# Performance work log

Measured on AMD Instinct MI355X. Metric: run time of the kernel, lower is better.

The kernel has to match this reference:

```python
import jax, jax.numpy as jnp
import numpy as np

B, C, N, L = 64, 32, 500, 12
C_OUT = 32
C_CAT = 9 * C  # (order*(support_len+1)+1)*c_in = 288


def setup_inputs() -> dict:
    key = jax.random.key(0)
    ks = jax.random.split(key, 7)
    x = jax.random.normal(ks[0], (B, C, N, L), dtype=jnp.float32)
    # row-stochastic-ish adjacencies: scale by 1/N to keep hops numerically tame
    A0 = jax.random.uniform(ks[1], (N, N), dtype=jnp.float32) / N
    A1 = jax.random.uniform(ks[2], (N, N), dtype=jnp.float32) / N
    A2 = jax.random.uniform(ks[3], (N, N), dtype=jnp.float32) / N
    A3 = jax.random.uniform(ks[4], (B, N, N), dtype=jnp.float32) / N
    W = jax.random.normal(ks[5], (C_OUT, C_CAT), dtype=jnp.float32) * 0.05
    b = jax.random.normal(ks[6], (C_OUT,), dtype=jnp.float32) * 0.05
    return {"x": x, "A0": A0, "A1": A1, "A2": A2, "A3": A3, "W": W, "b": b}


def reference(x, A0, A1, A2, A3, W, b):
    # x: [B, C, N, L]; A0..A2: [N, N]; A3: [B, N, N]; W: [C_OUT, 9*C]; b: [C_OUT]
    def hop2(h, A):  # static adjacency
        return jnp.einsum('ncvl,vw->ncwl', h, A)

    def hop3(h, A):  # batched (dynamic) adjacency
        return jnp.einsum('ncvl,nvw->ncwl', h, A)

    out = [x]
    for A in (A0, A1, A2):
        x1 = hop2(x, A)
        x2 = hop2(x1, A)
        out.extend([x1, x2])
    x1 = hop3(x, A3)
    x2 = hop3(x1, A3)
    out.extend([x1, x2])

    h = jnp.concatenate(out, axis=1)  # [B, 9C, N, L]
    # 1x1 Conv2d == channel mixing matmul + bias
    h = jnp.einsum('ncvl,oc->novl', h, W) + b[None, :, None, None]
    # dropout in eval mode: identity
    return h
```

## Files before the change

kernel.cpp:

```cpp
#include <hip/hip_runtime.h>

typedef unsigned short u16;
typedef __bf16 bf16x8 __attribute__((ext_vector_type(8)));
typedef float f32x4 __attribute__((ext_vector_type(4)));
typedef const unsigned int __attribute__((address_space(1))) gu32;
typedef unsigned int __attribute__((address_space(3))) lu32;

#define NN 500
#define LLc 12
#define CC 32
#define MM 384
#define KP 512
#define MT 96
#define NT2 128
#define XS_S 40
#define AS_S 40
#define CT2_S 136
#define TS_S 384
#define AT_ELS 256000

__device__ __forceinline__ u16 f2bf(float f) {
    union { float f; unsigned u; } cv; cv.f = f;
    unsigned u = cv.u;
    u += 0x7fffu + ((u >> 16) & 1u);
    return (u16)(u >> 16);
}
__device__ __forceinline__ float bf2f(u16 s) {
    union { unsigned u; float f; } cv; cv.u = ((unsigned)s) << 16;
    return cv.f;
}

__global__ __launch_bounds__(256) void atrans_all(
    const float* __restrict__ A0, const float* __restrict__ A1,
    const float* __restrict__ A2, const float* __restrict__ A3,
    u16* __restrict__ At_s, u16* __restrict__ At_b)
{
    __shared__ u16 Ls[32 * 36];
    const int t = threadIdx.x;
    const int n0 = blockIdx.x * 32;
    const int k0 = blockIdx.y * 32;
    const int z = blockIdx.z;
    const float* Ab; u16* Ob;
    if (z == 0)      { Ab = A0; Ob = At_s; }
    else if (z == 1) { Ab = A1; Ob = At_s + (long)AT_ELS; }
    else if (z == 2) { Ab = A2; Ob = At_s + 2L * AT_ELS; }
    else             { Ab = A3 + (long)(z - 3) * NN * NN; Ob = At_b + (long)(z - 3) * AT_ELS; }
    {
        int vl = t >> 3, u = t & 7;
        float4 v = make_float4(0.f, 0.f, 0.f, 0.f);
        if (k0 + vl < NN && n0 + 4 * u + 4 <= NN)
            v = *(const float4*)(Ab + (long)(k0 + vl) * NN + n0 + 4 * u);
        int nb = 4 * u;
        Ls[(nb + 0) * 36 + vl] = f2bf(v.x);
        Ls[(nb + 1) * 36 + vl] = f2bf(v.y);
        Ls[(nb + 2) * 36 + vl] = f2bf(v.z);
        Ls[(nb + 3) * 36 + vl] = f2bf(v.w);
    }
    __syncthreads();
    {
        int row = t >> 3, u = t & 7;
        if (n0 + row < NN)
            *(uint2*)(Ob + (long)(n0 + row) * KP + k0 + 4 * u) = *(const uint2*)(&Ls[row * 36 + 4 * u]);
    }
}

__global__ __launch_bounds__(256) void xpose_kernel(
    const float* __restrict__ x, u16* __restrict__ Xt)
{
    __shared__ u16 Ls[MM * 36];
    const int t = threadIdx.x;
    const int v0 = blockIdx.x * 32;
    const int b  = blockIdx.y;
    #pragma unroll
    for (int j = 0; j < 12; ++j) {
        int f = t + 256 * j;
        int c = f / 96;
        int r = f - c * 96;
        int vl = r / 3;
        int l3 = (r - vl * 3) * 4;
        float4 v = make_float4(0.f, 0.f, 0.f, 0.f);
        if (v0 + vl < NN)
            v = *(const float4*)(x + ((long)b * CC + c) * (NN * LLc) + (long)(v0 + vl) * LLc + l3);
        int mb = (c * LLc + l3) * 36 + vl;
        Ls[mb]       = f2bf(v.x);
        Ls[mb + 36]  = f2bf(v.y);
        Ls[mb + 72]  = f2bf(v.z);
        Ls[mb + 108] = f2bf(v.w);
    }
    __syncthreads();
    #pragma unroll
    for (int j = 0; j < 12; ++j) {
        int f = t + 256 * j;
        int row = f >> 3, u = f & 7;
        *(uint2*)(Xt + ((long)b * MM + row) * KP + v0 + 4 * u) = *(const uint2*)(&Ls[row * 36 + 4 * u]);
    }
}

__global__ __launch_bounds__(256) void wpack_kernel(
    const float* __restrict__ W, u16* __restrict__ Wp)
{
    const int t = threadIdx.x;
    #pragma unroll 1
    for (int k = 0; k < 72; ++k) {
        int idx = t + 256 * k;
        int j    = idx & 7;
        int lane = (idx >> 3) & 63;
        int p    = (idx >> 9) & 1;
        int mt   = (idx >> 10) & 1;
        int g    = idx >> 11;
        int o  = mt * 16 + (lane & 15);
        int kk = g * 32 + (lane >> 4) * 8 + j;
        float wv = W[o * 288 + kk];
        u16 hi = f2bf(wv);
        Wp[idx] = (p == 0) ? hi : f2bf(wv - bf2f(hi));
    }
}

__global__ __launch_bounds__(256, 3) void hop_fast4(
    const u16* __restrict__ Xsrc, long x_gstride, long x_bstride,
    const u16* __restrict__ At_s,
    const u16* __restrict__ At_b,
    u16* __restrict__ Hout, long h_gstride)
{
    __shared__ __align__(16) u16 smem[20480];
    u16* Ct = smem;

    const int t = threadIdx.x;
    const int lane = t & 63;
    const int wv = t >> 6;
    const int f0 = blockIdx.x + 4 * blockIdx.y + 8 * blockIdx.z;
    const int w  = (f0 & 7) * 256 + (f0 >> 3);
    const int bx = w & 3;
    const int by = (w >> 2) & 1;
    const int zc = w >> 3;
    const int g  = zc & 3;
    const int b  = zc >> 2;
    const int n0 = bx * NT2;
    const int m0 = by * 192;
    const int ln  = lane & 15;
    const int q16 = lane >> 4;

    const u16* Ab = (g < 3) ? (At_s + (long)g * AT_ELS) : (At_b + (long)b * AT_ELS);
    const u16* Xb = Xsrc + (long)g * x_gstride + (long)b * x_bstride;
    u16* Ob = Hout + (long)g * h_gstride + (long)b * ((long)MM * KP);

    const int rbase = lane >> 2;
    const int coff  = (((lane & 3) ^ ((lane >> 3) & 3)) << 3);
    const int rsel  = ((q16 ^ ((ln >> 1) & 3)) << 3);

    auto STAGE = [&](int kk, int pb) {
        #pragma unroll
        for (int j = 0; j < 5; ++j) {
            int o = (wv * 5 + j) << 10;
            const u16* src;
            if (o < 8192) {
                src = Ab + (long)(n0 + (o >> 6) + rbase) * KP + kk + coff;
            } else {
                src = Xb + (long)(m0 + (o >> 6) - 128 + rbase) * KP + kk + coff;
            }
            __builtin_amdgcn_global_load_lds((gu32*)src,
                (lu32*)((char*)smem + pb * 20480 + o), 16, 0, 0);
        }
    };

    f32x4 acc[2][12];
    #pragma unroll
    for (int ns = 0; ns < 2; ++ns)
        #pragma unroll
        for (int i = 0; i < 12; ++i)
            #pragma unroll
            for (int r = 0; r < 4; ++r) acc[ns][i][r] = 0.f;

    STAGE(0, 0);
    asm volatile("s_waitcnt vmcnt(0)" ::: "memory");
    __syncthreads();

    #pragma unroll 1
    for (int s = 0; s < 16; ++s) {
        const int pb = s & 1;
        if (s < 15) STAGE(32 * (s + 1), pb ^ 1);
        const u16* As = smem + pb * 10240;
        const u16* Xs = As + 4096;
        const int rowA0 = wv * 32 + ln;
        bf16x8 b0 = *(const bf16x8*)(&As[rowA0 * 32 + rsel]);
        bf16x8 b1 = *(const bf16x8*)(&As[(rowA0 + 16) * 32 + rsel]);
        #pragma unroll
        for (int i = 0; i < 12; ++i) {
            bf16x8 af = *(const bf16x8*)(&Xs[(i * 16 + ln) * 32 + rsel]);
            acc[0][i] = __builtin_amdgcn_mfma_f32_16x16x32_bf16(af, b0, acc[0][i], 0, 0, 0);
            acc[1][i] = __builtin_amdgcn_mfma_f32_16x16x32_bf16(af, b1, acc[1][i], 0, 0, 0);
        }
        asm volatile("s_waitcnt vmcnt(0)" ::: "memory");
        __syncthreads();
    }

    #pragma unroll
    for (int h = 0; h < 2; ++h) {
        __syncthreads();
        #pragma unroll
        for (int ns = 0; ns < 2; ++ns) {
            int col = wv * 32 + ns * 16 + ln;
            #pragma unroll
            for (int i6 = 0; i6 < 6; ++i6) {
                int rb = i6 * 16 + (lane >> 4) * 4;
                #pragma unroll
                for (int r = 0; r < 4; ++r)
                    Ct[(rb + r) * CT2_S + col] = f2bf(acc[ns][h * 6 + i6][r]);
            }
        }
        __syncthreads();
        #pragma unroll
        for (int j = 0; j < 12; ++j) {
            int f = t + 256 * j;
            int row = f >> 5, u = f & 31;
            int n = n0 + 4 * u;
            uint2 v = make_uint2(0u, 0u);
            if (n < NN) v = *(const uint2*)(&Ct[row * CT2_S + 4 * u]);
            *(uint2*)(Ob + (long)(m0 + h * 96 + row) * KP + n) = v;
        }
    }
}

__global__ __launch_bounds__(256, 3) void hop_fast3(
    const u16* __restrict__ Xsrc, long x_gstride, long x_bstride, int x_rstride, int x_klim,
    const u16* __restrict__ At_s,
    const u16* __restrict__ At_b,
    u16* __restrict__ Hout, long h_gstride)
{
    __shared__ __align__(16) u16 smem[13056];
    u16* As = smem;
    u16* Xs = smem + 5120;
    u16* Ct = smem;

    const int t = threadIdx.x;
    const int lane = t & 63;
    const int wv = t >> 6;
    const int f0 = blockIdx.x + 4 * blockIdx.y + 8 * blockIdx.z;
    const int w  = (f0 & 7) * 256 + (f0 >> 3);
    const int bx = w & 3;
    const int by = (w >> 2) & 1;
    const int zc = w >> 3;
    const int g  = zc & 3;
    const int b  = zc >> 2;
    const int n0 = bx * NT2;
    const int m0 = by * 192;
    const int ln = lane & 15;
    const int q8 = (lane >> 4) * 8;

    const u16* Ab = (g < 3) ? (At_s + (long)g * AT_ELS) : (At_b + (long)b * AT_ELS);
    const u16* Xb = Xsrc + (long)g * x_gstride + (long)b * x_bstride;
    u16* Ob = Hout + (long)g * h_gstride + (long)b * ((long)MM * NN);

    uint2 pa[4], px[6];
    auto loadA = [&](int k0) {
        #pragma unroll
        for (int j = 0; j < 4; ++j) {
            int f = t + 256 * j;
            int n = f >> 3, u = f & 7;
            uint2 v = make_uint2(0u, 0u);
            if (n0 + n < NN)
                v = *(const uint2*)(Ab + (long)(n0 + n) * KP + k0 + 4 * u);
            pa[j] = v;
        }
    };
    auto loadX = [&](int k0) {
        #pragma unroll
        for (int j = 0; j < 6; ++j) {
            int f = t + 256 * j;
            int r = f >> 3, u = f & 7;
            int k = k0 + 4 * u;
            uint2 v = make_uint2(0u, 0u);
            if (k < x_klim)
                v = *(const uint2*)(Xb + (long)(m0 + r) * x_rstride + k);
            px[j] = v;
        }
    };

    f32x4 acc[2][12];
    #pragma unroll
    for (int ns = 0; ns < 2; ++ns)
        #pragma unroll
        for (int i = 0; i < 12; ++i)
            #pragma unroll
            for (int r = 0; r < 4; ++r) acc[ns][i][r] = 0.f;

    loadA(0);
    loadX(0);
    #pragma unroll 1
    for (int s = 0; s < 16; ++s) {
        __syncthreads();
        #pragma unroll
        for (int j = 0; j < 4; ++j) {
            int f = t + 256 * j;
            *(uint2*)(&As[(f >> 3) * AS_S + 4 * (f & 7)]) = pa[j];
        }
        #pragma unroll
        for (int j = 0; j < 6; ++j) {
            int f = t + 256 * j;
            *(uint2*)(&Xs[(f >> 3) * XS_S + 4 * (f & 7)]) = px[j];
        }
        if (s < 15) {
            loadA(32 * (s + 1));
            loadX(32 * (s + 1));
        }
        __syncthreads();
        bf16x8 b0 = *(const bf16x8*)(&As[(wv * 32 + ln) * AS_S + q8]);
        bf16x8 b1 = *(const bf16x8*)(&As[(wv * 32 + 16 + ln) * AS_S + q8]);
        #pragma unroll
        for (int i = 0; i < 12; ++i) {
            bf16x8 af = *(const bf16x8*)(&Xs[(i * 16 + ln) * XS_S + q8]);
            acc[0][i] = __builtin_amdgcn_mfma_f32_16x16x32_bf16(af, b0, acc[0][i], 0, 0, 0);
            acc[1][i] = __builtin_amdgcn_mfma_f32_16x16x32_bf16(af, b1, acc[1][i], 0, 0, 0);
        }
    }

    #pragma unroll
    for (int h = 0; h < 2; ++h) {
        __syncthreads();
        #pragma unroll
        for (int ns = 0; ns < 2; ++ns) {
            int col = wv * 32 + ns * 16 + ln;
            #pragma unroll
            for (int i6 = 0; i6 < 6; ++i6) {
                int rb = i6 * 16 + (lane >> 4) * 4;
                #pragma unroll
                for (int r = 0; r < 4; ++r)
                    Ct[(rb + r) * CT2_S + col] = f2bf(acc[ns][h * 6 + i6][r]);
            }
        }
        __syncthreads();
        #pragma unroll
        for (int j = 0; j < 12; ++j) {
            int f = t + 256 * j;
            int row = f >> 5, u = f & 31;
            int n = n0 + 4 * u;
            if (n < NN)
                *(uint2*)(Ob + (long)(m0 + h * 96 + row) * NN + n) = *(const uint2*)(&Ct[row * CT2_S + 4 * u]);
        }
    }
}

__global__ __launch_bounds__(512, 4) void mix_mfma(
    const u16* __restrict__ Xt,
    const u16* __restrict__ H,
    const u16* __restrict__ Wp,
    const float* __restrict__ bias,
    float* __restrict__ out,
    long h_gs, long h_bs, int h_rs)
{
    __shared__ __align__(16) char smem[50176];
    u16*   Ls = (u16*)smem;
    float* Ct = (float*)smem;

    const int t   = threadIdx.x;
    const int wg  = blockIdx.y * 8 + blockIdx.x;
    const int swz = (wg & 7) * 64 + (wg >> 3);
    const int bx  = swz & 7;
    const int b   = swz >> 3;
    const int n0  = bx * 64;
    const int w    = t >> 6;
    const int lane = t & 63;
    const int kq   = lane >> 4;
    const int ln   = lane & 15;
    const int srow   = lane >> 3;
    const int schunk = (lane & 7) * 8;

    f32x4 acc[6][2];
    #pragma unroll
    for (int i = 0; i < 6; ++i)
        #pragma unroll
        for (int m = 0; m < 2; ++m)
            #pragma unroll
            for (int r = 0; r < 4; ++r) acc[i][m][r] = 0.f;

    #pragma unroll 1
    for (int g = 0; g < 9; ++g) {
        const u16* base; int rs;
        if (g == 0) { base = Xt + (long)b * (MM * KP); rs = KP; }
        else {
            int gg = g - 1;
            int buf = (gg & 1) ? 4 + (gg >> 1) : (gg >> 1);
            base = H + (long)buf * h_gs + (long)b * h_bs; rs = h_rs;
        }
        __syncthreads();
        #pragma unroll
        for (int i = 0; i < 6; ++i) {
            int r0 = (w * 6 + i) * 8;
            const u16* src = base + (long)(r0 + srow) * rs + n0 + schunk;
            __builtin_amdgcn_global_load_lds((gu32*)src, (lu32*)(Ls + r0 * 64), 16, 0, 0);
        }
        asm volatile("s_waitcnt vmcnt(0)" ::: "memory");
        __syncthreads();
        uint4 wf[2][2];
        #pragma unroll
        for (int mt = 0; mt < 2; ++mt)
            #pragma unroll
            for (int p = 0; p < 2; ++p)
                wf[mt][p] = *(const uint4*)(Wp + ((((g * 2 + mt) * 2 + p) * 64 + lane) * 8));
        #pragma unroll
        for (int i = 0; i < 6; ++i) {
            int ct = w * 6 + i;
            int off0 = kq * 6144 + (ct >> 2) * 64 + (ct & 3) * 16 + ln;
            union { u16 s[8]; bf16x8 v; } fb;
            #pragma unroll
            for (int j = 0; j < 8; ++j) fb.s[j] = Ls[off0 + j * 768];
            #pragma unroll
            for (int mt = 0; mt < 2; ++mt) {
                acc[i][mt] = __builtin_amdgcn_mfma_f32_16x16x32_bf16(*(const bf16x8*)&wf[mt][0], fb.v, acc[i][mt], 0, 0, 0);
                acc[i][mt] = __builtin_amdgcn_mfma_f32_16x16x32_bf16(*(const bf16x8*)&wf[mt][1], fb.v, acc[i][mt], 0, 0, 0);
            }
        }
    }

    #pragma unroll
    for (int mt = 0; mt < 2; ++mt) {
        __syncthreads();
        #pragma unroll
        for (int i = 0; i < 6; ++i) {
            int col = (w * 6 + i) * 16 + ln;
            #pragma unroll
            for (int r = 0; r < 4; ++r)
                Ct[(kq * 4 + r) * 781 + col] = acc[i][mt][r];
        }
        __syncthreads();
        int o16 = t >> 5, u = t & 31;
        int og = mt * 16 + o16;
        float bs = bias[og];
        float* ob = out + (((long)b * CC + og) * NN + n0) * 12L;
        #pragma unroll
        for (int j2 = 0; j2 < 2; ++j2) {
            int n = u + 32 * j2;
            if (n0 + n < NN) {
                float v[12];
                #pragma unroll
                for (int l = 0; l < 12; ++l) v[l] = Ct[o16 * 781 + l * 64 + n] + bs;
                #pragma unroll
                for (int q = 0; q < 3; ++q)
                    *(float4*)(ob + (long)n * 12 + q * 4) = *(const float4*)&v[q * 4];
            }
        }
    }
}

__global__ __launch_bounds__(256, 3) void mix_all(
    const u16* __restrict__ Xt,
    const u16* __restrict__ H,
    const float* __restrict__ W,
    const float* __restrict__ bias,
    float* __restrict__ out)
{
    __shared__ __align__(16) float smem[96 * 36 + 288 * 33];
    float* ts = smem;
    float* Ws = smem + 96 * 36;

    const int t  = threadIdx.x;
    const int b  = blockIdx.y;
    const int w0 = blockIdx.x * 32;
    const int o  = t & 31;
    const int wq = t >> 5;
    const int w4 = wq * 4;
    const long HBUF = (long)64 * MM * NN;

    #pragma unroll
    for (int j = 0; j < 36; ++j) {
        int f = t + 256 * j;
        int oo = f & 31, ci = f >> 5;
        Ws[ci * 33 + oo] = W[oo * 288 + ci];
    }

    float acc[4][12];
    #pragma unroll
    for (int k = 0; k < 4; ++k)
        #pragma unroll
        for (int l = 0; l < 12; ++l) acc[k][l] = 0.f;

    uint2 px[3];
    auto loadq = [&](int q) {
        int g = q >> 2, c0 = (q & 3) << 3;
        const u16* base; int rs;
        if (g == 0) { base = Xt + (long)b * (MM * KP); rs = KP; }
        else {
            int gg = g - 1, i = gg >> 1;
            int buf = (gg & 1) ? 4 + i : i;
            base = H + (long)buf * HBUF + (long)b * ((long)MM * NN); rs = NN;
        }
        int m0c = c0 * 12;
        #pragma unroll
        for (int j = 0; j < 3; ++j) {
            int f = t + 256 * j;
            int r = f >> 3, u = f & 7;
            px[j] = *(const uint2*)(base + (long)(m0c + r) * rs + w0 + 4 * u);
        }
    };

    loadq(0);
    #pragma unroll 1
    for (int q = 0; q < 36; ++q) {
        __syncthreads();
        #pragma unroll
        for (int j = 0; j < 3; ++j) {
            int f = t + 256 * j;
            int r = f >> 3, u = f & 7;
            uint2 raw = px[j];
            float4 v = make_float4(bf2f((u16)(raw.x & 0xffffu)), bf2f((u16)(raw.x >> 16)),
                                   bf2f((u16)(raw.y & 0xffffu)), bf2f((u16)(raw.y >> 16)));
            *(float4*)(&ts[r * 36 + 4 * u]) = v;
        }
        if (q < 35) loadq(q + 1);
        __syncthreads();
        int g = q >> 2, c0 = (q & 3) << 3;
        #pragma unroll 1
        for (int cl = 0; cl < 8; ++cl) {
            float wgt = Ws[(g * 32 + c0 + cl) * 33 + o];
            #pragma unroll
            for (int l = 0; l < 12; ++l) {
                float4 h = *(const float4*)(&ts[(cl * 12 + l) * 36 + w4]);
                acc[0][l] += wgt * h.x;
                acc[1][l] += wgt * h.y;
                acc[2][l] += wgt * h.z;
                acc[3][l] += wgt * h.w;
            }
        }
    }

    #pragma unroll 1
    for (int r = 0; r < 4; ++r) {
        __syncthreads();
        if ((o >> 3) == r) {
            int ol = o & 7;
            #pragma unroll
            for (int k = 0; k < 4; ++k)
                #pragma unroll
                for (int l = 0; l < 12; ++l)
                    ts[ol * 388 + (w4 + k) * 12 + l] = acc[k][l];
        }
        __syncthreads();
        #pragma unroll
        for (int j = 0; j < 3; ++j) {
            int f4 = t + 256 * j;
            int ol = f4 / 96;
            int rem = f4 - ol * 96;
            int w  = rem / 3;
            int lq = rem - w * 3;
            if (w0 + w < NN) {
                float4 v = *(const float4*)(&ts[ol * 388 + w * 12 + lq * 4]);
                float bs = bias[r * 8 + ol];
                v.x += bs; v.y += bs; v.z += bs; v.w += bs;
                *(float4*)(out + (((long)b * CC + r * 8 + ol) * NN + w0 + w) * LLc + lq * 4) = v;
            }
        }
    }
}

__global__ __launch_bounds__(256, 4) void hop_fast(
    const u16* __restrict__ Xsrc, long x_bstride, int x_rstride, int x_klim,
    const u16* __restrict__ At,   long a_bstride,
    u16* __restrict__ hout)
{
    __shared__ __align__(16) u16 smem[13056];
    u16* As = smem;
    u16* Xs = smem + 5120;
    u16* Ct = smem;

    const int t = threadIdx.x;
    const int lane = t & 63;
    const int wv = t >> 6;
    const int n0 = blockIdx.x * NT2;
    const int m0 = blockIdx.y * MT;
    const int b  = blockIdx.z;
    const int ln = lane & 15;
    const int q8 = (lane >> 4) * 8;

    const u16* Ab = At + (long)b * a_bstride;
    const u16* Xb = Xsrc + (long)b * x_bstride;

    uint2 pa[4], px[3];
    auto loadA = [&](int k0) {
        #pragma unroll
        for (int j = 0; j < 4; ++j) {
            int f = t + 256 * j;
            int n = f >> 3, u = f & 7;
            uint2 v = make_uint2(0u, 0u);
            if (n0 + n < NN)
                v = *(const uint2*)(Ab + (long)(n0 + n) * KP + k0 + 4 * u);
            pa[j] = v;
        }
    };
    auto loadX = [&](int k0) {
        #pragma unroll
        for (int j = 0; j < 3; ++j) {
            int f = t + 256 * j;
            int r = f >> 3, u = f & 7;
            int k = k0 + 4 * u;
            uint2 v = make_uint2(0u, 0u);
            if (k < x_klim)
                v = *(const uint2*)(Xb + (long)(m0 + r) * x_rstride + k);
            px[j] = v;
        }
    };

    f32x4 acc[2][6];
    #pragma unroll
    for (int ns = 0; ns < 2; ++ns)
        #pragma unroll
        for (int i = 0; i < 6; ++i)
            #pragma unroll
            for (int r = 0; r < 4; ++r) acc[ns][i][r] = 0.f;

    loadA(0);
    loadX(0);
    #pragma unroll 1
    for (int s = 0; s < 16; ++s) {
        __syncthreads();
        #pragma unroll
        for (int j = 0; j < 4; ++j) {
            int f = t + 256 * j;
            *(uint2*)(&As[(f >> 3) * AS_S + 4 * (f & 7)]) = pa[j];
        }
        #pragma unroll
        for (int j = 0; j < 3; ++j) {
            int f = t + 256 * j;
            *(uint2*)(&Xs[(f >> 3) * XS_S + 4 * (f & 7)]) = px[j];
        }
        if (s < 15) {
            loadA(32 * (s + 1));
            loadX(32 * (s + 1));
        }
        __syncthreads();
        bf16x8 af[6];
        #pragma unroll
        for (int i = 0; i < 6; ++i)
            af[i] = *(const bf16x8*)(&Xs[(i * 16 + ln) * XS_S + q8]);
        #pragma unroll
        for (int ns = 0; ns < 2; ++ns) {
            bf16x8 bfr = *(const bf16x8*)(&As[(wv * 32 + ns * 16 + ln) * AS_S + q8]);
            #pragma unroll
            for (int i = 0; i < 6; ++i)
                acc[ns][i] = __builtin_amdgcn_mfma_f32_16x16x32_bf16(af[i], bfr, acc[ns][i], 0, 0, 0);
        }
    }

    __syncthreads();
    #pragma unroll
    for (int ns = 0; ns < 2; ++ns) {
        int col = wv * 32 + ns * 16 + ln;
        #pragma unroll
        for (int i = 0; i < 6; ++i) {
            int rb = i * 16 + (lane >> 4) * 4;
            #pragma unroll
            for (int r = 0; r < 4; ++r)
                Ct[(rb + r) * CT2_S + col] = f2bf(acc[ns][i][r]);
        }
    }
    __syncthreads();
    u16* Ob = hout + (long)b * ((long)MM * NN);
    #pragma unroll
    for (int j = 0; j < 12; ++j) {
        int f = t + 256 * j;
        int row = f >> 5, u = f & 31;
        int n = n0 + 4 * u;
        if (n < NN)
            *(uint2*)(Ob + (long)(m0 + row) * NN + n) = *(const uint2*)(&Ct[row * CT2_S + 4 * u]);
    }
}

__global__ __launch_bounds__(256, 2) void mix_kernel(
    const float* __restrict__ x,
    const u16* __restrict__ h1,
    const u16* __restrict__ h2,
    const float* __restrict__ W,
    const float* __restrict__ bias,
    int blk1, int blk2,
    float* __restrict__ out, int init)
{
    __shared__ __align__(16) float smem[CC * TS_S + 3 * 1056];
    float* ts = smem;
    float* Ws = smem + CC * TS_S;

    const int t = threadIdx.x;
    const int b = blockIdx.y;
    const int w0 = blockIdx.x * 32;
    const int o  = t & 15;
    const int wg = (t >> 4) & 7;
    const int lh = t >> 7;

    #pragma unroll
    for (int j = 0; j < 4; ++j) {
        int f = t + 256 * j;
        int oo = f & 31, c = f >> 5;
        Ws[c * 33 + oo]        = W[oo * 288 + blk1 * 32 + c];
        Ws[1056 + c * 33 + oo] = W[oo * 288 + blk2 * 32 + c];
        if (init) Ws[2112 + c * 33 + oo] = W[oo * 288 + c];
    }

    float acc2[2][4][6];
    #pragma unroll
    for (int a = 0; a < 2; ++a)
        #pragma unroll
        for (int q = 0; q < 4; ++q)
            #pragma unroll
            for (int l = 0; l < 6; ++l) acc2[a][q][l] = 0.f;

    auto stage_h = [&](const u16* h) {
        #pragma unroll
        for (int j = 0; j < 12; ++j) {
            int f = t + 256 * j;
            int row = f >> 3, u = f & 7;
            int w = w0 + 4 * u;
            uint2 raw = make_uint2(0u, 0u);
            if (w < NN)
                raw = *(const uint2*)(h + ((long)b * MM + row) * NN + w);
            int c = row / 12;
            int l = row - c * 12;
            float* dst = &ts[c * TS_S + l * 32 + 4 * u];
            dst[0] = bf2f((u16)(raw.x & 0xffffu));
            dst[1] = bf2f((u16)(raw.x >> 16));
            dst[2] = bf2f((u16)(raw.y & 0xffffu));
            dst[3] = bf2f((u16)(raw.y >> 16));
        }
    };
    auto accum = [&](const float* Wg) {
        for (int c = 0; c < CC; ++c) {
            float w1 = Wg[c * 33 + o];
            float w2 = Wg[c * 33 + o + 16];
            #pragma unroll
            for (int l6 = 0; l6 < 6; ++l6) {
                const float4 hv = *(const float4*)(&ts[c * TS_S + (lh * 6 + l6) * 32 + wg * 4]);
                acc2[0][0][l6] += w1 * hv.x;
                acc2[0][1][l6] += w1 * hv.y;
                acc2[0][2][l6] += w1 * hv.z;
                acc2[0][3][l6] += w1 * hv.w;
                acc2[1][0][l6] += w2 * hv.x;
                acc2[1][1][l6] += w2 * hv.y;
                acc2[1][2][l6] += w2 * hv.z;
                acc2[1][3][l6] += w2 * hv.w;
            }
        }
    };

    if (init) {
        #pragma unroll
        for (int j = 0; j < 12; ++j) {
            int f = t + 256 * j;
            int c = f / 96;
            int r = f - c * 96;
            int w = r / 3;
            int q = r - w * 3;
            float4 v = make_float4(0.f, 0.f, 0.f, 0.f);
            if (w0 + w < NN)
                v = *(const float4*)(x + ((long)b * CC + c) * (NN * LLc) + (long)(w0 + w) * LLc + q * 4);
            float* dst = &ts[c * TS_S + (q * 4) * 32 + w];
            dst[0]  = v.x; dst[32] = v.y; dst[64] = v.z; dst[96] = v.w;
        }
        __syncthreads();
        accum(Ws + 2112);
        __syncthreads();
    }
    stage_h(h1);
    __syncthreads();
    accum(Ws);
    __syncthreads();
    stage_h(h2);
    __syncthreads();
    accum(Ws + 1056);

    #pragma unroll
    for (int oh = 0; oh < 2; ++oh) {
        int oo = o + 16 * oh;
        float bs = init ? bias[oo] : 0.f;
        #pragma unroll
        for (int q = 0; q < 4; ++q) {
            int w = w0 + wg * 4 + q;
            if (w < NN) {
                float* op = out + ((long)b * CC + oo) * (NN * LLc) + (long)w * LLc + lh * 6;
                #pragma unroll
                for (int p = 0; p < 3; ++p) {
                    float2* pp = (float2*)op + p;
                    float2 v;
                    if (init) {
                        v.x = bs + acc2[oh][q][2 * p];
                        v.y = bs + acc2[oh][q][2 * p + 1];
                    } else {
                        v = *pp;
                        v.x += acc2[oh][q][2 * p];
                        v.y += acc2[oh][q][2 * p + 1];
                    }
                    *pp = v;
                }
            }
        }
    }
}

extern "C" void kernel_launch(void* const* d_in, const int* in_sizes, int n_in,
                              void* d_out, int out_size, void* d_ws, size_t ws_size,
                              hipStream_t stream) {
    const float* x    = (const float*)d_in[0];
    const float* A0   = (const float*)d_in[1];
    const float* A1   = (const float*)d_in[2];
    const float* A2   = (const float*)d_in[3];
    const float* A3   = (const float*)d_in[4];
    const float* W    = (const float*)d_in[5];
    const float* bias = (const float*)d_in[6];
    float* out = (float*)d_out;
    char* ws = (char*)d_ws;

    const size_t HBUF_ELS  = (size_t)64 * MM * NN;
    const size_t H8_BYTES  = 8 * HBUF_ELS * 2;
    const size_t AT_BYTES  = (size_t)AT_ELS * 2;
    const size_t A3T_BYTES = 64 * AT_BYTES;
    const size_t XT_BYTES  = (size_t)64 * MM * KP * 2;
    const size_t need2 = H8_BYTES + 3 * AT_BYTES + A3T_BYTES + XT_BYTES;
    const size_t WPK_BYTES = 36864;
    const size_t need3 = need2 + WPK_BYTES;
    const size_t HB2_ELS  = (size_t)64 * MM * KP;
    const size_t H8B_PAD  = 8 * HB2_ELS * 2;
    const size_t need4 = H8B_PAD + 3 * AT_BYTES + A3T_BYTES + XT_BYTES + WPK_BYTES;

    dim3 blk(256);
    dim3 hgrid(4, 2, 256);

    if (ws_size >= need4) {
        u16* Hb   = (u16*)ws;
        u16* At_s = (u16*)(ws + H8B_PAD);
        u16* A3t  = At_s + 3L * AT_ELS;
        u16* Xt   = (u16*)(ws + H8B_PAD + 3 * AT_BYTES + A3T_BYTES);
        u16* Wpk  = Xt + (size_t)64 * MM * KP;

        atrans_all<<<dim3(16, 16, 67), blk, 0, stream>>>(A0, A1, A2, A3, At_s, A3t);
        xpose_kernel<<<dim3(16, 64), blk, 0, stream>>>(x, Xt);
        wpack_kernel<<<dim3(1), blk, 0, stream>>>(W, Wpk);
        hop_fast4<<<hgrid, blk, 0, stream>>>(
            Xt, 0L, (long)MM * KP, At_s, A3t, Hb, (long)HB2_ELS);
        hop_fast4<<<hgrid, blk, 0, stream>>>(
            Hb, (long)HB2_ELS, (long)MM * KP, At_s, A3t,
            Hb + 4 * HB2_ELS, (long)HB2_ELS);
        mix_mfma<<<dim3(8, 64), dim3(512), 0, stream>>>(
            Xt, Hb, Wpk, bias, out, (long)HB2_ELS, (long)MM * KP, KP);
        return;
    }

    if (ws_size >= need3) {
        u16* Hb   = (u16*)ws;
        u16* At_s = (u16*)(ws + H8_BYTES);
        u16* A3t  = At_s + 3L * AT_ELS;
        u16* Xt   = (u16*)(ws + H8_BYTES + 3 * AT_BYTES + A3T_BYTES);
        u16* Wpk  = (u16*)(ws + need2);

        atrans_all<<<dim3(16, 16, 67), blk, 0, stream>>>(A0, A1, A2, A3, At_s, A3t);
        xpose_kernel<<<dim3(16, 64), blk, 0, stream>>>(x, Xt);
        wpack_kernel<<<dim3(1), blk, 0, stream>>>(W, Wpk);
        hop_fast3<<<hgrid, blk, 0, stream>>>(
            Xt, 0L, (long)MM * KP, KP, KP, At_s, A3t, Hb, (long)HBUF_ELS);
        hop_fast3<<<hgrid, blk, 0, stream>>>(
            Hb, (long)HBUF_ELS, (long)MM * NN, NN, NN, At_s, A3t,
            Hb + 4 * HBUF_ELS, (long)HBUF_ELS);
        mix_mfma<<<dim3(8, 64), dim3(512), 0, stream>>>(
            Xt, Hb, Wpk, bias, out, (long)HBUF_ELS, (long)MM * NN, NN);
        return;
    }

    if (ws_size >= need2) {
        u16* H    = (u16*)ws;
        u16* At_s = (u16*)(ws + H8_BYTES);
        u16* A3t  = At_s + 3L * AT_ELS;
        u16* Xt   = (u16*)(ws + H8_BYTES + 3 * AT_BYTES + A3T_BYTES);

        atrans_all<<<dim3(16, 16, 67), blk, 0, stream>>>(A0, A1, A2, A3, At_s, A3t);
        xpose_kernel<<<dim3(16, 64), blk, 0, stream>>>(x, Xt);
        hop_fast3<<<hgrid, blk, 0, stream>>>(
            Xt, 0L, (long)MM * KP, KP, KP, At_s, A3t, H, (long)HBUF_ELS);
        hop_fast3<<<hgrid, blk, 0, stream>>>(
            H, (long)HBUF_ELS, (long)MM * NN, NN, NN, At_s, A3t,
            H + 4 * HBUF_ELS, (long)HBUF_ELS);
        mix_all<<<dim3(16, 64), blk, 0, stream>>>(Xt, H, W, bias, out);
        return;
    }

    const size_t H_BYTES   = HBUF_ELS * 2;
    const size_t need_at   = 2 * H_BYTES + 3 * AT_BYTES + A3T_BYTES;

    u16* H1 = (u16*)ws;
    u16* H2 = (u16*)(ws + H_BYTES);
    u16* At0 = (u16*)(ws + 2 * H_BYTES);
    u16* A3t = At0 + 3L * AT_ELS;
    u16* Xt  = (u16*)(ws + need_at);

    dim3 fgrid(4, 4, 64);
    dim3 mgrid(16, 64);

    xpose_kernel<<<dim3(16, 64), blk, 0, stream>>>(x, Xt);
    atrans_all<<<dim3(16, 16, 67), blk, 0, stream>>>(A0, A1, A2, A3, At0, A3t);

    const long XT_BS = (long)MM * KP;
    const long H_BS  = (long)MM * NN;
    u16* Atp[4] = {At0, At0 + (long)AT_ELS, At0 + 2L * AT_ELS, A3t};

    for (int i = 0; i < 4; ++i) {
        long a_bs = (i == 3) ? (long)AT_ELS : 0;
        hop_fast<<<fgrid, blk, 0, stream>>>(Xt, XT_BS, KP, KP, Atp[i], a_bs, H1);
        hop_fast<<<fgrid, blk, 0, stream>>>(H1, H_BS, NN, NN, Atp[i], a_bs, H2);
        mix_kernel<<<mgrid, blk, 0, stream>>>(i == 0 ? x : nullptr, H1, H2, W, bias,
                                              2 * i + 1, 2 * i + 2, out, i == 0 ? 1 : 0);
    }
}
```

Baseline: 370.8 us.

## Triple-buffer hop kernel LDS pipeline and parallelize weight packing

The hop GEMM kernel moves from a double-buffered to a triple-buffered global-to-LDS pipeline. It prefetches two stages ahead, waits with a partial vmcnt, and uses one barrier per iteration instead of two, with MFMA sections raised to higher wave priority. LDS grows to 60KB per block, so launch bounds drop from 3 to 2 blocks per CU, which lowers occupancy in exchange for deeper latency hiding. Separately, the weight-packing kernel is spread across 72 blocks instead of one serial block, to cut its launch-critical latency.

Measured after the change: 374.2 us. About the same (+0.9%).

```diff
diff --git a/kernel.cpp b/kernel.cpp
--- a/kernel.cpp
+++ b/kernel.cpp
@@ -99,30 +99,26 @@
 __global__ __launch_bounds__(256) void wpack_kernel(
     const float* __restrict__ W, u16* __restrict__ Wp)
 {
-    const int t = threadIdx.x;
-    #pragma unroll 1
-    for (int k = 0; k < 72; ++k) {
-        int idx = t + 256 * k;
-        int j    = idx & 7;
-        int lane = (idx >> 3) & 63;
-        int p    = (idx >> 9) & 1;
-        int mt   = (idx >> 10) & 1;
-        int g    = idx >> 11;
-        int o  = mt * 16 + (lane & 15);
-        int kk = g * 32 + (lane >> 4) * 8 + j;
-        float wv = W[o * 288 + kk];
-        u16 hi = f2bf(wv);
-        Wp[idx] = (p == 0) ? hi : f2bf(wv - bf2f(hi));
-    }
-}
-
-__global__ __launch_bounds__(256, 3) void hop_fast4(
+    int idx = blockIdx.x * 256 + threadIdx.x;
+    int j    = idx & 7;
+    int lane = (idx >> 3) & 63;
+    int p    = (idx >> 9) & 1;
+    int mt   = (idx >> 10) & 1;
+    int g    = idx >> 11;
+    int o  = mt * 16 + (lane & 15);
+    int kk = g * 32 + (lane >> 4) * 8 + j;
+    float wv = W[o * 288 + kk];
+    u16 hi = f2bf(wv);
+    Wp[idx] = (p == 0) ? hi : f2bf(wv - bf2f(hi));
+}
+
+__global__ __launch_bounds__(256, 2) void hop_fast5(
     const u16* __restrict__ Xsrc, long x_gstride, long x_bstride,
     const u16* __restrict__ At_s,
     const u16* __restrict__ At_b,
     u16* __restrict__ Hout, long h_gstride)
 {
-    __shared__ __align__(16) u16 smem[20480];
+    __shared__ __align__(16) u16 smem[30720];
     u16* Ct = smem;
 
     const int t = threadIdx.x;
@@ -171,28 +167,38 @@
             #pragma unroll
             for (int r = 0; r < 4; ++r) acc[ns][i][r] = 0.f;
 
-    STAGE(0, 0);
-    asm volatile("s_waitcnt vmcnt(0)" ::: "memory");
-    __syncthreads();
-
-    #pragma unroll 1
-    for (int s = 0; s < 16; ++s) {
-        const int pb = s & 1;
-        if (s < 15) STAGE(32 * (s + 1), pb ^ 1);
+    auto COMPUTE = [&](int pb) {
         const u16* As = smem + pb * 10240;
         const u16* Xs = As + 4096;
         const int rowA0 = wv * 32 + ln;
         bf16x8 b0 = *(const bf16x8*)(&As[rowA0 * 32 + rsel]);
         bf16x8 b1 = *(const bf16x8*)(&As[(rowA0 + 16) * 32 + rsel]);
+        __builtin_amdgcn_s_setprio(1);
         #pragma unroll
         for (int i = 0; i < 12; ++i) {
             bf16x8 af = *(const bf16x8*)(&Xs[(i * 16 + ln) * 32 + rsel]);
             acc[0][i] = __builtin_amdgcn_mfma_f32_16x16x32_bf16(af, b0, acc[0][i], 0, 0, 0);
             acc[1][i] = __builtin_amdgcn_mfma_f32_16x16x32_bf16(af, b1, acc[1][i], 0, 0, 0);
         }
-        asm volatile("s_waitcnt vmcnt(0)" ::: "memory");
-        __syncthreads();
-    }
+        __builtin_amdgcn_s_setprio(0);
+    };
+
+    STAGE(0, 0);
+    STAGE(32, 1);
+    int c0 = 0, c1 = 1, c2 = 2;
+    #pragma unroll 1
+    for (int s = 0; s < 15; ++s) {
+        asm volatile("s_waitcnt vmcnt(5)" ::: "memory");
+        __builtin_amdgcn_s_barrier();
+        __builtin_amdgcn_sched_barrier(0);
+        if (s <= 13) STAGE(32 * (s + 2), c2);
+        COMPUTE(c0);
+        int tmp = c0; c0 = c1; c1 = c2; c2 = tmp;
+    }
+    asm volatile("s_waitcnt vmcnt(0)" ::: "memory");
+    __builtin_amdgcn_s_barrier();
+    __builtin_amdgcn_sched_barrier(0);
+    COMPUTE(c0);
 
     #pragma unroll
     for (int h = 0; h < 2; ++h) {
@@ -829,10 +835,10 @@
 
         atrans_all<<<dim3(16, 16, 67), blk, 0, stream>>>(A0, A1, A2, A3, At_s, A3t);
         xpose_kernel<<<dim3(16, 64), blk, 0, stream>>>(x, Xt);
-        wpack_kernel<<<dim3(1), blk, 0, stream>>>(W, Wpk);
-        hop_fast4<<<hgrid, blk, 0, stream>>>(
+        wpack_kernel<<<dim3(72), blk, 0, stream>>>(W, Wpk);
+        hop_fast5<<<hgrid, blk, 0, stream>>>(
             Xt, 0L, (long)MM * KP, At_s, A3t, Hb, (long)HB2_ELS);
-        hop_fast4<<<hgrid, blk, 0, stream>>>(
+        hop_fast5<<<hgrid, blk, 0, stream>>>(
             Hb, (long)HB2_ELS, (long)MM * KP, At_s, A3t,
             Hb + 4 * HB2_ELS, (long)HB2_ELS);
         mix_mfma<<<dim3(8, 64), dim3(512), 0, stream>>>(
@@ -849,7 +855,7 @@
 
         atrans_all<<<dim3(16, 16, 67), blk, 0, stream>>>(A0, A1, A2, A3, At_s, A3t);
         xpose_kernel<<<dim3(16, 64), blk, 0, stream>>>(x, Xt);
-        wpack_kernel<<<dim3(1), blk, 0, stream>>>(W, Wpk);
+        wpack_kernel<<<dim3(72), blk, 0, stream>>>(W, Wpk);
         hop_fast3<<<hgrid, blk, 0, stream>>>(
             Xt, 0L, (long)MM * KP, KP, KP, At_s, A3t, Hb, (long)HBUF_ELS);
         hop_fast3<<<hgrid, blk, 0, stream>>>(
```

## Fuse prep kernels into one launch and shrink hop tiles to 128x128

Applied to the files above, without the earlier changes.

Merges the adjacency transpose, x transpose and weight packing into a single prep_all launch, and spreads weight packing across many blocks instead of one serial block. The hop GEMM kernel moves from 192x128 tiles to 128x128 tiles, giving 12 tiles per batch-group instead of 8, a smaller LDS footprint and a launch bound of 4 blocks per SM. This should cut launch overhead and raise occupancy and parallelism. The cost is less reuse of each staged adjacency tile and more redundant adjacency loads.

After: 362.1 us. 2.3% less time.

```diff
diff --git a/kernel.cpp b/kernel.cpp
--- a/kernel.cpp
+++ b/kernel.cpp
@@ -28,6 +28,87 @@
 __device__ __forceinline__ float bf2f(u16 s) {
     union { unsigned u; float f; } cv; cv.u = ((unsigned)s) << 16;
     return cv.f;
+}
+
+__global__ __launch_bounds__(256) void prep_all(
+    const float* __restrict__ x,
+    const float* __restrict__ A0, const float* __restrict__ A1,
+    const float* __restrict__ A2, const float* __restrict__ A3,
+    u16* __restrict__ At_s, u16* __restrict__ At_b,
+    u16* __restrict__ Xt,
+    const float* __restrict__ W, u16* __restrict__ Wp)
+{
+    __shared__ u16 Ls[MM * 36];
+    const int id = blockIdx.x;
+    const int t = threadIdx.x;
+
+    if (id < 17152) {
+        int rem = id & 255;
+        int z  = id >> 8;
+        int n0 = (rem & 15) * 32;
+        int k0 = (rem >> 4) * 32;
+        const float* Ab; u16* Ob;
+        if (z == 0)      { Ab = A0; Ob = At_s; }
+        else if (z == 1) { Ab = A1; Ob = At_s + (long)AT_ELS; }
+        else if (z == 2) { Ab = A2; Ob = At_s + 2L * AT_ELS; }
+        else             { Ab = A3 + (long)(z - 3) * NN * NN; Ob = At_b + (long)(z - 3) * AT_ELS; }
+        {
+            int vl = t >> 3, u = t & 7;
+            float4 v = make_float4(0.f, 0.f, 0.f, 0.f);
+            if (k0 + vl < NN && n0 + 4 * u + 4 <= NN)
+                v = *(const float4*)(Ab + (long)(k0 + vl) * NN + n0 + 4 * u);
+            int nb = 4 * u;
+            Ls[(nb + 0) * 36 + vl] = f2bf(v.x);
+            Ls[(nb + 1) * 36 + vl] = f2bf(v.y);
+            Ls[(nb + 2) * 36 + vl] = f2bf(v.z);
+            Ls[(nb + 3) * 36 + vl] = f2bf(v.w);
+        }
+        __syncthreads();
+        {
+            int row = t >> 3, u = t & 7;
+            if (n0 + row < NN)
+                *(uint2*)(Ob + (long)(n0 + row) * KP + k0 + 4 * u) = *(const uint2*)(&Ls[row * 36 + 4 * u]);
+        }
+    } else if (id < 18176) {
+        int jj = id - 17152;
+        int v0 = (jj & 15) * 32;
+        int b  = jj >> 4;
+        #pragma unroll
+        for (int j = 0; j < 12; ++j) {
+            int f = t + 256 * j;
+            int c = f / 96;
+            int r = f - c * 96;
+            int vl = r / 3;
+            int l3 = (r - vl * 3) * 4;
+            float4 v = make_float4(0.f, 0.f, 0.f, 0.f);
+            if (v0 + vl < NN)
+                v = *(const float4*)(x + ((long)b * CC + c) * (NN * LLc) + (long)(v0 + vl) * LLc + l3);
+            int mb = (c * LLc + l3) * 36 + vl;
+            Ls[mb]       = f2bf(v.x);
+            Ls[mb + 36]  = f2bf(v.y);
+            Ls[mb + 72]  = f2bf(v.z);
+            Ls[mb + 108] = f2bf(v.w);
+        }
+        __syncthreads();
+        #pragma unroll
+        for (int j = 0; j < 12; ++j) {
+            int f = t + 256 * j;
+            int row = f >> 3, u = f & 7;
+            *(uint2*)(Xt + ((long)b * MM + row) * KP + v0 + 4 * u) = *(const uint2*)(&Ls[row * 36 + 4 * u]);
+        }
+    } else {
+        int idx = (id - 18176) * 256 + t;
+        int j    = idx & 7;
+        int lane = (idx >> 3) & 63;
+        int p    = (idx >> 9) & 1;
+        int mt   = (idx >> 10) & 1;
+        int g    = idx >> 11;
+        int o  = mt * 16 + (lane & 15);
+        int kk = g * 32 + (lane >> 4) * 8 + j;
+        float wv = W[o * 288 + kk];
+        u16 hi = f2bf(wv);
+        Wp[idx] = (p == 0) ? hi : f2bf(wv - bf2f(hi));
+    }
 }
 
 __global__ __launch_bounds__(256) void atrans_all(
@@ -99,44 +180,41 @@
 __global__ __launch_bounds__(256) void wpack_kernel(
     const float* __restrict__ W, u16* __restrict__ Wp)
 {
-    const int t = threadIdx.x;
-    #pragma unroll 1
-    for (int k = 0; k < 72; ++k) {
-        int idx = t + 256 * k;
-        int j    = idx & 7;
-        int lane = (idx >> 3) & 63;
-        int p    = (idx >> 9) & 1;
-        int mt   = (idx >> 10) & 1;
-        int g    = idx >> 11;
-        int o  = mt * 16 + (lane & 15);
-        int kk = g * 32 + (lane >> 4) * 8 + j;
-        float wv = W[o * 288 + kk];
-        u16 hi = f2bf(wv);
-        Wp[idx] = (p == 0) ? hi : f2bf(wv - bf2f(hi));
-    }
-}
-
-__global__ __launch_bounds__(256, 3) void hop_fast4(
+    int idx = blockIdx.x * 256 + threadIdx.x;
+    int j    = idx & 7;
+    int lane = (idx >> 3) & 63;
+    int p    = (idx >> 9) & 1;
+    int mt   = (idx >> 10) & 1;
+    int g    = idx >> 11;
+    int o  = mt * 16 + (lane & 15);
+    int kk = g * 32 + (lane >> 4) * 8 + j;
+    float wv = W[o * 288 + kk];
+    u16 hi = f2bf(wv);
+    Wp[idx] = (p == 0) ? hi : f2bf(wv - bf2f(hi));
+}
+
+__global__ __launch_bounds__(256, 4) void hop_fast6(
     const u16* __restrict__ Xsrc, long x_gstride, long x_bstride,
     const u16* __restrict__ At_s,
     const u16* __restrict__ At_b,
     u16* __restrict__ Hout, long h_gstride)
 {
-    __shared__ __align__(16) u16 smem[20480];
+    __shared__ __align__(16) u16 smem[16384];
     u16* Ct = smem;
 
     const int t = threadIdx.x;
     const int lane = t & 63;
     const int wv = t >> 6;
-    const int f0 = blockIdx.x + 4 * blockIdx.y + 8 * blockIdx.z;
-    const int w  = (f0 & 7) * 256 + (f0 >> 3);
-    const int bx = w & 3;
-    const int by = (w >> 2) & 1;
-    const int zc = w >> 3;
+    const int f0 = blockIdx.x + 4 * (blockIdx.y + 3 * blockIdx.z);
+    const int w  = (f0 & 7) * 384 + (f0 >> 3);
+    const int zc = w / 12;
+    const int rem = w - zc * 12;
+    const int bx = rem & 3;
+    const int by = rem >> 2;
     const int g  = zc & 3;
     const int b  = zc >> 2;
-    const int n0 = bx * NT2;
-    const int m0 = by * 192;
+    const int n0 = bx * 128;
+    const int m0 = by * 128;
     const int ln  = lane & 15;
     const int q16 = lane >> 4;
 
@@ -150,8 +228,8 @@
 
     auto STAGE = [&](int kk, int pb) {
         #pragma unroll
-        for (int j = 0; j < 5; ++j) {
-            int o = (wv * 5 + j) << 10;
+        for (int j = 0; j < 4; ++j) {
+            int o = (wv * 4 + j) << 10;
             const u16* src;
             if (o < 8192) {
                 src = Ab + (long)(n0 + (o >> 6) + rbase) * KP + kk + coff;
@@ -159,15 +237,15 @@
                 src = Xb + (long)(m0 + (o >> 6) - 128 + rbase) * KP + kk + coff;
             }
             __builtin_amdgcn_global_load_lds((gu32*)src,
-                (lu32*)((char*)smem + pb * 20480 + o), 16, 0, 0);
+                (lu32*)((char*)smem + pb * 16384 + o), 16, 0, 0);
         }
     };
 
-    f32x4 acc[2][12];
+    f32x4 acc[2][8];
     #pragma unroll
     for (int ns = 0; ns < 2; ++ns)
         #pragma unroll
-        for (int i = 0; i < 12; ++i)
+        for (int i = 0; i < 8; ++i)
             #pragma unroll
             for (int r = 0; r < 4; ++r) acc[ns][i][r] = 0.f;
 
@@ -179,13 +257,12 @@
     for (int s = 0; s < 16; ++s) {
         const int pb = s & 1;
         if (s < 15) STAGE(32 * (s + 1), pb ^ 1);
-        const u16* As = smem + pb * 10240;
+        const u16* As = smem + pb * 8192;
         const u16* Xs = As + 4096;
-        const int rowA0 = wv * 32 + ln;
-        bf16x8 b0 = *(const bf16x8*)(&As[rowA0 * 32 + rsel]);
-        bf16x8 b1 = *(const bf16x8*)(&As[(rowA0 + 16) * 32 + rsel]);
-        #pragma unroll
-        for (int i = 0; i < 12; ++i) {
+        bf16x8 b0 = *(const bf16x8*)(&As[(wv * 32 + ln) * 32 + rsel]);
+        bf16x8 b1 = *(const bf16x8*)(&As[(wv * 32 + 16 + ln) * 32 + rsel]);
+        #pragma unroll
+        for (int i = 0; i < 8; ++i) {
             bf16x8 af = *(const bf16x8*)(&Xs[(i * 16 + ln) * 32 + rsel]);
             acc[0][i] = __builtin_amdgcn_mfma_f32_16x16x32_bf16(af, b0, acc[0][i], 0, 0, 0);
             acc[1][i] = __builtin_amdgcn_mfma_f32_16x16x32_bf16(af, b1, acc[1][i], 0, 0, 0);
@@ -201,22 +278,22 @@
         for (int ns = 0; ns < 2; ++ns) {
             int col = wv * 32 + ns * 16 + ln;
             #pragma unroll
-            for (int i6 = 0; i6 < 6; ++i6) {
-                int rb = i6 * 16 + (lane >> 4) * 4;
+            for (int i4 = 0; i4 < 4; ++i4) {
+                int rb = i4 * 16 + (lane >> 4) * 4;
                 #pragma unroll
                 for (int r = 0; r < 4; ++r)
-                    Ct[(rb + r) * CT2_S + col] = f2bf(acc[ns][h * 6 + i6][r]);
+                    Ct[(rb + r) * CT2_S + col] = f2bf(acc[ns][h * 4 + i4][r]);
             }
         }
         __syncthreads();
         #pragma unroll
-        for (int j = 0; j < 12; ++j) {
+        for (int j = 0; j < 8; ++j) {
             int f = t + 256 * j;
             int row = f >> 5, u = f & 31;
             int n = n0 + 4 * u;
             uint2 v = make_uint2(0u, 0u);
             if (n < NN) v = *(const uint2*)(&Ct[row * CT2_S + 4 * u]);
-            *(uint2*)(Ob + (long)(m0 + h * 96 + row) * KP + n) = v;
+            *(uint2*)(Ob + (long)(m0 + h * 64 + row) * KP + n) = v;
         }
     }
 }
@@ -818,7 +895,6 @@
     const size_t need4 = H8B_PAD + 3 * AT_BYTES + A3T_BYTES + XT_BYTES + WPK_BYTES;
 
     dim3 blk(256);
-    dim3 hgrid(4, 2, 256);
 
     if (ws_size >= need4) {
         u16* Hb   = (u16*)ws;
@@ -827,18 +903,18 @@
         u16* Xt   = (u16*)(ws + H8B_PAD + 3 * AT_BYTES + A3T_BYTES);
         u16* Wpk  = Xt + (size_t)64 * MM * KP;
 
-        atrans_all<<<dim3(16, 16, 67), blk, 0, stream>>>(A0, A1, A2, A3, At_s, A3t);
-        xpose_kernel<<<dim3(16, 64), blk, 0, stream>>>(x, Xt);
-        wpack_kernel<<<dim3(1), blk, 0, stream>>>(W, Wpk);
-        hop_fast4<<<hgrid, blk, 0, stream>>>(
+        prep_all<<<dim3(18248), blk, 0, stream>>>(x, A0, A1, A2, A3, At_s, A3t, Xt, W, Wpk);
+        hop_fast6<<<dim3(4, 3, 256), blk, 0, stream>>>(
             Xt, 0L, (long)MM * KP, At_s, A3t, Hb, (long)HB2_ELS);
-        hop_fast4<<<hgrid, blk, 0, stream>>>(
+        hop_fast6<<<dim3(4, 3, 256), blk, 0, stream>>>(
             Hb, (long)HB2_ELS, (long)MM * KP, At_s, A3t,
             Hb + 4 * HB2_ELS, (long)HB2_ELS);
         mix_mfma<<<dim3(8, 64), dim3(512), 0, stream>>>(
             Xt, Hb, Wpk, bias, out, (long)HB2_ELS, (long)MM * KP, KP);
         return;
     }
+
+    dim3 hgrid(4, 2, 256);
 
     if (ws_size >= need3) {
         u16* Hb   = (u16*)ws;
@@ -849,7 +925,7 @@
 
         atrans_all<<<dim3(16, 16, 67), blk, 0, stream>>>(A0, A1, A2, A3, At_s, A3t);
         xpose_kernel<<<dim3(16, 64), blk, 0, stream>>>(x, Xt);
-        wpack_kernel<<<dim3(1), blk, 0, stream>>>(W, Wpk);
+        wpack_kernel<<<dim3(72), blk, 0, stream>>>(W, Wpk);
         hop_fast3<<<hgrid, blk, 0, stream>>>(
             Xt, 0L, (long)MM * KP, KP, KP, At_s, A3t, Hb, (long)HBUF_ELS);
         hop_fast3<<<hgrid, blk, 0, stream>>>(
```
